# Kernel tuning notes

Measured on AMD Instinct MI355X. Metric: run time of the kernel, lower is better.

## Reference

```python
import jax, jax.numpy as jnp
import numpy as np

N_NODES = 100000
N_EDGES = 1600000
IN_C, HID_C, OUT_C = 128, 256, 47


def setup_inputs() -> dict:
    key = jax.random.key(0)
    ks = jax.random.split(key, 8)
    x = jax.random.normal(ks[0], (N_NODES, IN_C), dtype=jnp.float32)
    edge_index = jax.random.randint(ks[1], (2, N_EDGES), 0, N_NODES, dtype=jnp.int64)

    def glorot(k, fan_in, fan_out):
        s = 1.0 / np.sqrt(fan_in)
        return jax.random.uniform(k, (fan_in, fan_out), jnp.float32, -s, s)

    W1_l = glorot(ks[2], IN_C, HID_C)
    b1 = jnp.zeros((HID_C,), jnp.float32)
    W1_r = glorot(ks[3], IN_C, HID_C)
    W2_l = glorot(ks[4], HID_C, OUT_C)
    b2 = jnp.zeros((OUT_C,), jnp.float32)
    W2_r = glorot(ks[5], HID_C, OUT_C)
    return {"x": x, "edge_index": edge_index,
            "W1_l": W1_l, "b1": b1, "W1_r": W1_r,
            "W2_l": W2_l, "b2": b2, "W2_r": W2_r}


def _sage_conv(x, src, dst, W_l, b, W_r, num_nodes):
    # mean aggregation of source-node features onto destination nodes
    msg_sum = jax.ops.segment_sum(x[src], dst, num_segments=num_nodes)  # [N, C]
    cnt = jax.ops.segment_sum(jnp.ones((src.shape[0], 1), x.dtype), dst,
                              num_segments=num_nodes)                   # [N, 1]
    mean = msg_sum / jnp.maximum(cnt, 1.0)
    # out = lin_l(mean) + lin_r(x_root); lin_l carries the bias (PyG default)
    return mean @ W_l + b + x @ W_r


def reference(x, edge_index, W1_l, b1, W1_r, W2_l, b2, W2_r):
    num_nodes = x.shape[0]
    src, dst = edge_index[0], edge_index[1]
    h = _sage_conv(x, src, dst, W1_l, b1, W1_r, num_nodes)
    h = jax.nn.relu(h)  # dropout is identity in eval mode
    out = _sage_conv(h, src, dst, W2_l, b2, W2_r, num_nodes)
    return jax.nn.log_softmax(out, axis=-1)
```

## Files before the change

### kernel.cpp

```cpp
#include <hip/hip_runtime.h>
#include <hip/hip_bf16.h>

constexpr int IN_C  = 128;
constexpr int HID_C = 256;
constexpr int OUT_C = 47;
constexpr int CAP   = 64;

typedef __attribute__((ext_vector_type(8))) short bf16x8;
typedef __attribute__((ext_vector_type(4))) float f32x4;

static __device__ __forceinline__ unsigned short f2bf(float v) {
  __hip_bfloat16 hb = __float2bfloat16(v);
  return *(unsigned short*)&hb;
}
static __device__ __forceinline__ float bf2f(unsigned short u) {
  return __uint_as_float((unsigned)u << 16);
}

__global__ __launch_bounds__(256) void fill_bucket(const int* __restrict__ src,
                                                   const int* __restrict__ dst,
                                                   int* __restrict__ cursor,
                                                   int* __restrict__ csr,
                                                   int E, int lo, int hi) {
  int e = blockIdx.x * blockDim.x + threadIdx.x;
  const int stride = gridDim.x * blockDim.x;
  for (; e < E; e += stride) {
    const int d = __builtin_nontemporal_load(&dst[e]);
    if (d >= lo && d < hi) {
      const int s = __builtin_nontemporal_load(&src[e]);
      const int p = atomicAdd(&cursor[d], 1);
      if (p < CAP) csr[(size_t)d * CAP + p] = s;
    }
  }
}

__global__ void f32_to_bf16(const float* __restrict__ in, unsigned short* __restrict__ out, int n4) {
  int i = blockIdx.x * blockDim.x + threadIdx.x;
  if (i < n4) {
    float4 v = *(const float4*)&in[i * 4];
    ushort4 o;
    o.x = f2bf(v.x); o.y = f2bf(v.y); o.z = f2bf(v.z); o.w = f2bf(v.w);
    *(ushort4*)&out[i * 4] = o;
  }
}

__global__ void build_weights(const float* __restrict__ W1l, const float* __restrict__ W1r,
                              const float* __restrict__ W2l, const float* __restrict__ W2r,
                              unsigned short* __restrict__ W1T, unsigned short* __restrict__ W2T) {
  int idx = blockIdx.x * blockDim.x + threadIdx.x;
  if (idx < 256 * 256) {
    int j = idx >> 8, k = idx & 255;
    float v = (k < 128) ? W1l[k * 256 + j] : W1r[(k - 128) * 256 + j];
    W1T[idx] = f2bf(v);
  } else if (idx < 256 * 256 + 128 * 256) {
    int t = idx - 256 * 256;
    int j = t >> 8, k = t & 255;
    float v = 0.f;
    if (j < OUT_C)           v = W2l[k * OUT_C + j];
    else if (j < 2 * OUT_C)  v = W2r[k * OUT_C + (j - OUT_C)];
    W2T[t] = f2bf(v);
  }
}

__global__ __launch_bounds__(256) void agg1(const unsigned short* __restrict__ xb,
                                            const int* __restrict__ cursor,
                                            const int* __restrict__ csr,
                                            unsigned short* __restrict__ meanb, int N) {
  const int wid  = (blockIdx.x * blockDim.x + threadIdx.x) >> 6;
  const int lane = threadIdx.x & 63;
  if (wid >= N) return;
  const unsigned* xw = (const unsigned*)xb;
  const int degr = cursor[wid];
  const int deg  = min(degr, CAP);
  const int idx  = (lane < deg) ? csr[(size_t)wid * CAP + lane] : 0;
  float a0 = 0.f, a1 = 0.f, b0 = 0.f, b1 = 0.f;
  float c0 = 0.f, c1 = 0.f, d0 = 0.f, d1 = 0.f;
  int e = 0;
  for (; e + 4 <= deg; e += 4) {
    const int sA = __shfl(idx, e, 64),     sB = __shfl(idx, e + 1, 64);
    const int sC = __shfl(idx, e + 2, 64), sD = __shfl(idx, e + 3, 64);
    const unsigned uA = xw[(size_t)sA * 64 + lane];
    const unsigned uB = xw[(size_t)sB * 64 + lane];
    const unsigned uC = xw[(size_t)sC * 64 + lane];
    const unsigned uD = xw[(size_t)sD * 64 + lane];
    a0 += __uint_as_float(uA << 16); a1 += __uint_as_float(uA & 0xffff0000u);
    b0 += __uint_as_float(uB << 16); b1 += __uint_as_float(uB & 0xffff0000u);
    c0 += __uint_as_float(uC << 16); c1 += __uint_as_float(uC & 0xffff0000u);
    d0 += __uint_as_float(uD << 16); d1 += __uint_as_float(uD & 0xffff0000u);
  }
  for (; e < deg; ++e) {
    const int sA = __shfl(idx, e, 64);
    const unsigned uA = xw[(size_t)sA * 64 + lane];
    a0 += __uint_as_float(uA << 16); a1 += __uint_as_float(uA & 0xffff0000u);
  }
  const float r0 = (a0 + b0) + (c0 + d0);
  const float r1 = (a1 + b1) + (c1 + d1);
  const float inv = (degr > 0) ? 1.0f / (float)degr : 0.0f;
  const unsigned lo = f2bf(r0 * inv), hi = f2bf(r1 * inv);
  ((unsigned*)meanb)[(size_t)wid * 64 + lane] = lo | (hi << 16);
}

template<int MODE>
__global__ __launch_bounds__(256) void gemm_mfma(const unsigned short* __restrict__ A0,
                                                 const unsigned short* __restrict__ A1,
                                                 const unsigned short* __restrict__ BT,
                                                 const float* __restrict__ bias,
                                                 unsigned short* __restrict__ Out,
                                                 int M) {
  constexpr int ONC = (MODE == 0) ? 256 : 128;
  __shared__ unsigned short Asl[128 * 64];
  __shared__ unsigned short Bsl[128 * 64];
  const int tid  = threadIdx.x;
  const int wid  = tid >> 6, lane = tid & 63;
  const int wm   = wid >> 1, wn = wid & 1;
  const int r0   = blockIdx.x * 128;
  const int c0   = blockIdx.y * 128;

  f32x4 acc[4][4];
  #pragma unroll
  for (int m = 0; m < 4; ++m)
    #pragma unroll
    for (int n = 0; n < 4; ++n)
      #pragma unroll
      for (int j = 0; j < 4; ++j) acc[m][n][j] = 0.f;

  const int srow = lane >> 3;
  const int cs   = (lane & 7) ^ srow;
  const int fr   = lane & 15;
  const int klo  = (lane >> 4) * 16;
  const int swz  = (fr & 7) << 4;

  #pragma unroll 1
  for (int kb = 0; kb < 4; ++kb) {
    const unsigned short* Ap;
    int acol, ak;
    if (MODE == 0) { Ap = (kb < 2) ? A0 : A1; acol = (kb & 1) * 64; ak = 128; }
    else           { Ap = A0;                 acol = kb * 64;       ak = 256; }
    #pragma unroll
    for (int i = 0; i < 4; ++i) {
      const int rl = wid * 32 + i * 8 + srow;
      int gr = r0 + rl; if (gr > M - 1) gr = M - 1;
      const unsigned short* gsa = Ap + (size_t)gr * ak + acol + cs * 8;
      __builtin_amdgcn_global_load_lds(
          (const __attribute__((address_space(1))) unsigned int*)gsa,
          (__attribute__((address_space(3))) unsigned int*)&Asl[(wid * 32 + i * 8) * 64],
          16, 0, 0);
      const unsigned short* gsb = BT + (size_t)(c0 + rl) * 256 + kb * 64 + cs * 8;
      __builtin_amdgcn_global_load_lds(
          (const __attribute__((address_space(1))) unsigned int*)gsb,
          (__attribute__((address_space(3))) unsigned int*)&Bsl[(wid * 32 + i * 8) * 64],
          16, 0, 0);
    }
    asm volatile("s_waitcnt vmcnt(0)");
    __syncthreads();
    #pragma unroll
    for (int ks = 0; ks < 2; ++ks) {
      bf16x8 af[4], bfv[4];
      #pragma unroll
      for (int m = 0; m < 4; ++m) {
        const int ro = (wm * 64 + m * 16 + fr) * 128 + ((ks * 64 + klo) ^ swz);
        af[m] = *(const bf16x8*)((const char*)Asl + ro);
      }
      #pragma unroll
      for (int n = 0; n < 4; ++n) {
        const int ro = (wn * 64 + n * 16 + fr) * 128 + ((ks * 64 + klo) ^ swz);
        bfv[n] = *(const bf16x8*)((const char*)Bsl + ro);
      }
      #pragma unroll
      for (int m = 0; m < 4; ++m)
        #pragma unroll
        for (int n = 0; n < 4; ++n)
          acc[m][n] = __builtin_amdgcn_mfma_f32_16x16x32_bf16(af[m], bfv[n], acc[m][n], 0, 0, 0);
    }
    __syncthreads();
  }

  const int orow0 = r0 + wm * 64 + (lane >> 4) * 4;
  const int ocol0 = c0 + wn * 64 + (lane & 15);
  #pragma unroll
  for (int m = 0; m < 4; ++m) {
    #pragma unroll
    for (int n = 0; n < 4; ++n) {
      const int col = ocol0 + n * 16;
      const float badd = (MODE == 0) ? bias[col] : 0.f;
      #pragma unroll
      for (int j = 0; j < 4; ++j) {
        const int row = orow0 + m * 16 + j;
        if (row < M) {
          float v = acc[m][n][j] + badd;
          if (MODE == 0) v = fmaxf(v, 0.f);
          Out[(size_t)row * ONC + col] = f2bf(v);
        }
      }
    }
  }
}

__global__ __launch_bounds__(256) void final_kernel(const unsigned short* __restrict__ Ob,
                                                    const int* __restrict__ cursor,
                                                    const int* __restrict__ csr,
                                                    const float* __restrict__ b2,
                                                    float* __restrict__ out, int N) {
  const int wid  = (blockIdx.x * blockDim.x + threadIdx.x) >> 6;
  const int lane = threadIdx.x & 63;
  if (wid >= N) return;
  const int degr = cursor[wid];
  const int deg  = min(degr, CAP);
  const int idx  = (lane < deg) ? csr[(size_t)wid * CAP + lane] : 0;
  const bool act = lane < OUT_C;
  const int cl = act ? lane : 0;
  float t0 = 0.f, t1 = 0.f, t2 = 0.f, t3 = 0.f;
  int e = 0;
  for (; e + 4 <= deg; e += 4) {
    const int sA = __shfl(idx, e, 64),     sB = __shfl(idx, e + 1, 64);
    const int sC = __shfl(idx, e + 2, 64), sD = __shfl(idx, e + 3, 64);
    if (act) {
      t0 += bf2f(Ob[(size_t)sA * 128 + lane]);
      t1 += bf2f(Ob[(size_t)sB * 128 + lane]);
      t2 += bf2f(Ob[(size_t)sC * 128 + lane]);
      t3 += bf2f(Ob[(size_t)sD * 128 + lane]);
    }
  }
  for (; e < deg; ++e) {
    const int sA = __shfl(idx, e, 64);
    if (act) t0 += bf2f(Ob[(size_t)sA * 128 + lane]);
  }
  const float sum = (t0 + t1) + (t2 + t3);
  const float inv = (degr > 0) ? 1.0f / (float)degr : 0.0f;
  float v = sum * inv + b2[cl] + bf2f(Ob[(size_t)wid * 128 + OUT_C + cl]);
  if (!act) v = -INFINITY;
  float m = v;
  #pragma unroll
  for (int o = 32; o > 0; o >>= 1) m = fmaxf(m, __shfl_xor(m, o, 64));
  float ex = act ? expf(v - m) : 0.f;
  float s = ex;
  #pragma unroll
  for (int o = 32; o > 0; o >>= 1) s += __shfl_xor(s, o, 64);
  if (act) out[(size_t)wid * OUT_C + lane] = v - m - logf(s);
}


extern "C" void kernel_launch(void* const* d_in, const int* in_sizes, int n_in,
                              void* d_out, int out_size, void* d_ws, size_t ws_size,
                              hipStream_t stream) {
  const float* x   = (const float*)d_in[0];
  const int*   ei  = (const int*)d_in[1];
  const float* W1l = (const float*)d_in[2];
  const float* b1  = (const float*)d_in[3];
  const float* W1r = (const float*)d_in[4];
  const float* W2l = (const float*)d_in[5];
  const float* b2  = (const float*)d_in[6];
  const float* W2r = (const float*)d_in[7];
  float* out = (float*)d_out;

  const int N = in_sizes[0] / IN_C;
  const int E = in_sizes[1] / 2;
  const int* src = ei;
  const int* dst = ei + E;

  char* base = (char*)d_ws;
  size_t o = 0;
  auto take = [&](size_t bytes) -> char* {
    char* p = base + o;
    o = (o + bytes + 255) & ~(size_t)255;
    return p;
  };
  int* cursor = (int*)take((size_t)N * 4);
  const size_t zero_bytes = o;
  int* csr    = (int*)take((size_t)N * CAP * 4);
  unsigned short* xb    = (unsigned short*)take((size_t)N * IN_C * 2);
  unsigned short* meanb = (unsigned short*)take((size_t)N * IN_C * 2);
  unsigned short* h     = (unsigned short*)take((size_t)N * HID_C * 2);
  unsigned short* W1T   = (unsigned short*)take((size_t)256 * 256 * 2);
  unsigned short* W2T   = (unsigned short*)take((size_t)128 * 256 * 2);
  unsigned short* Ocat  = meanb;
  (void)ws_size; (void)n_in; (void)out_size;

  hipMemsetAsync(base, 0, zero_bytes, stream);

  const int tb = 256;

  const int P = 8;
  const int chunk = (N + P - 1) / P;
  for (int p = 0; p < P; ++p) {
    const int lo = p * chunk;
    const int hi = min(N, lo + chunk);
    fill_bucket<<<2048, tb, 0, stream>>>(src, dst, cursor, csr, E, lo, hi);
  }

  const int n4 = N * IN_C / 4;
  f32_to_bf16<<<(n4 + tb - 1) / tb, tb, 0, stream>>>(x, xb, n4);
  build_weights<<<384, 256, 0, stream>>>(W1l, W1r, W2l, W2r, W1T, W2T);

  agg1<<<(N + 3) / 4, 256, 0, stream>>>(xb, cursor, csr, meanb, N);

  const int mb = (N + 127) / 128;
  gemm_mfma<0><<<dim3(mb, 2), 256, 0, stream>>>(meanb, xb, W1T, b1, h, N);
  gemm_mfma<1><<<dim3(mb, 1), 256, 0, stream>>>(h, nullptr, W2T, nullptr, Ocat, N);

  final_kernel<<<(N + 3) / 4, 256, 0, stream>>>(Ocat, cursor, csr, b2, out, N);
}
```

Before: 425.6 us.

## Split layer-2 GEMM output into separate 64-wide arrays and unroll gathers by eight

The second GEMM now writes two 64-column arrays instead of one 128-wide array: the neighbour-projected part (W2_l) and the root part (W2_r). The W2 weight columns are re-laid out to match. The final gather now reads 128-byte rows from a compact array, which improves cache-line density for the random neighbour reads. Both gather loops (agg1 and final) are also unrolled to eight loads in flight, to raise memory-level parallelism at the cost of more registers.

Result: faster. 409.5 us (-3.8%).

```diff
diff --git a/kernel.cpp b/kernel.cpp
--- a/kernel.cpp
+++ b/kernel.cpp
@@ -16,6 +16,8 @@
 static __device__ __forceinline__ float bf2f(unsigned short u) {
   return __uint_as_float((unsigned)u << 16);
 }
+static __device__ __forceinline__ float lof(unsigned u) { return __uint_as_float(u << 16); }
+static __device__ __forceinline__ float hif(unsigned u) { return __uint_as_float(u & 0xffff0000u); }
 
 __global__ __launch_bounds__(256) void fill_bucket(const int* __restrict__ src,
                                                    const int* __restrict__ dst,
@@ -56,8 +58,8 @@
     int t = idx - 256 * 256;
     int j = t >> 8, k = t & 255;
     float v = 0.f;
-    if (j < OUT_C)           v = W2l[k * OUT_C + j];
-    else if (j < 2 * OUT_C)  v = W2r[k * OUT_C + (j - OUT_C)];
+    if (j < OUT_C)                     v = W2l[k * OUT_C + j];
+    else if (j >= 64 && j < 64 + OUT_C) v = W2r[k * OUT_C + (j - 64)];
     W2T[t] = f2bf(v);
   }
 }
@@ -76,28 +78,38 @@
   float a0 = 0.f, a1 = 0.f, b0 = 0.f, b1 = 0.f;
   float c0 = 0.f, c1 = 0.f, d0 = 0.f, d1 = 0.f;
   int e = 0;
+  for (; e + 8 <= deg; e += 8) {
+    const int s0 = __shfl(idx, e, 64),     s1 = __shfl(idx, e + 1, 64);
+    const int s2 = __shfl(idx, e + 2, 64), s3 = __shfl(idx, e + 3, 64);
+    const int s4 = __shfl(idx, e + 4, 64), s5 = __shfl(idx, e + 5, 64);
+    const int s6 = __shfl(idx, e + 6, 64), s7 = __shfl(idx, e + 7, 64);
+    const unsigned u0 = xw[(size_t)s0 * 64 + lane], u1 = xw[(size_t)s1 * 64 + lane];
+    const unsigned u2 = xw[(size_t)s2 * 64 + lane], u3 = xw[(size_t)s3 * 64 + lane];
+    const unsigned u4 = xw[(size_t)s4 * 64 + lane], u5 = xw[(size_t)s5 * 64 + lane];
+    const unsigned u6 = xw[(size_t)s6 * 64 + lane], u7 = xw[(size_t)s7 * 64 + lane];
+    a0 += lof(u0); a1 += hif(u0); b0 += lof(u1); b1 += hif(u1);
+    c0 += lof(u2); c1 += hif(u2); d0 += lof(u3); d1 += hif(u3);
+    a0 += lof(u4); a1 += hif(u4); b0 += lof(u5); b1 += hif(u5);
+    c0 += lof(u6); c1 += hif(u6); d0 += lof(u7); d1 += hif(u7);
+  }
   for (; e + 4 <= deg; e += 4) {
-    const int sA = __shfl(idx, e, 64),     sB = __shfl(idx, e + 1, 64);
-    const int sC = __shfl(idx, e + 2, 64), sD = __shfl(idx, e + 3, 64);
-    const unsigned uA = xw[(size_t)sA * 64 + lane];
-    const unsigned uB = xw[(size_t)sB * 64 + lane];
-    const unsigned uC = xw[(size_t)sC * 64 + lane];
-    const unsigned uD = xw[(size_t)sD * 64 + lane];
-    a0 += __uint_as_float(uA << 16); a1 += __uint_as_float(uA & 0xffff0000u);
-    b0 += __uint_as_float(uB << 16); b1 += __uint_as_float(uB & 0xffff0000u);
-    c0 += __uint_as_float(uC << 16); c1 += __uint_as_float(uC & 0xffff0000u);
-    d0 += __uint_as_float(uD << 16); d1 += __uint_as_float(uD & 0xffff0000u);
+    const int s0 = __shfl(idx, e, 64),     s1 = __shfl(idx, e + 1, 64);
+    const int s2 = __shfl(idx, e + 2, 64), s3 = __shfl(idx, e + 3, 64);
+    const unsigned u0 = xw[(size_t)s0 * 64 + lane], u1 = xw[(size_t)s1 * 64 + lane];
+    const unsigned u2 = xw[(size_t)s2 * 64 + lane], u3 = xw[(size_t)s3 * 64 + lane];
+    a0 += lof(u0); a1 += hif(u0); b0 += lof(u1); b1 += hif(u1);
+    c0 += lof(u2); c1 += hif(u2); d0 += lof(u3); d1 += hif(u3);
   }
   for (; e < deg; ++e) {
-    const int sA = __shfl(idx, e, 64);
-    const unsigned uA = xw[(size_t)sA * 64 + lane];
-    a0 += __uint_as_float(uA << 16); a1 += __uint_as_float(uA & 0xffff0000u);
+    const int s0 = __shfl(idx, e, 64);
+    const unsigned u0 = xw[(size_t)s0 * 64 + lane];
+    a0 += lof(u0); a1 += hif(u0);
   }
   const float r0 = (a0 + b0) + (c0 + d0);
   const float r1 = (a1 + b1) + (c1 + d1);
   const float inv = (degr > 0) ? 1.0f / (float)degr : 0.0f;
-  const unsigned lo = f2bf(r0 * inv), hi = f2bf(r1 * inv);
-  ((unsigned*)meanb)[(size_t)wid * 64 + lane] = lo | (hi << 16);
+  const unsigned wlo = f2bf(r0 * inv), whi = f2bf(r1 * inv);
+  ((unsigned*)meanb)[(size_t)wid * 64 + lane] = wlo | (whi << 16);
 }
 
 template<int MODE>
@@ -106,8 +118,8 @@
                                                  const unsigned short* __restrict__ BT,
                                                  const float* __restrict__ bias,
                                                  unsigned short* __restrict__ Out,
+                                                 unsigned short* __restrict__ OutR,
                                                  int M) {
-  constexpr int ONC = (MODE == 0) ? 256 : 128;
   __shared__ unsigned short Asl[128 * 64];
   __shared__ unsigned short Bsl[128 * 64];
   const int tid  = threadIdx.x;
@@ -188,15 +200,21 @@
         const int row = orow0 + m * 16 + j;
         if (row < M) {
           float v = acc[m][n][j] + badd;
-          if (MODE == 0) v = fmaxf(v, 0.f);
-          Out[(size_t)row * ONC + col] = f2bf(v);
+          if (MODE == 0) {
+            v = fmaxf(v, 0.f);
+            Out[(size_t)row * HID_C + col] = f2bf(v);
+          } else {
+            if (col < 64) Out[(size_t)row * 64 + col] = f2bf(v);
+            else          OutR[(size_t)row * 64 + (col - 64)] = f2bf(v);
+          }
         }
       }
     }
   }
 }
 
-__global__ __launch_bounds__(256) void final_kernel(const unsigned short* __restrict__ Ob,
+__global__ __launch_bounds__(256) void final_kernel(const unsigned short* __restrict__ Ol,
+                                                    const unsigned short* __restrict__ Or,
                                                     const int* __restrict__ cursor,
                                                     const int* __restrict__ csr,
                                                     const float* __restrict__ b2,
@@ -211,23 +229,39 @@
   const int cl = act ? lane : 0;
   float t0 = 0.f, t1 = 0.f, t2 = 0.f, t3 = 0.f;
   int e = 0;
+  for (; e + 8 <= deg; e += 8) {
+    const int s0 = __shfl(idx, e, 64),     s1 = __shfl(idx, e + 1, 64);
+    const int s2 = __shfl(idx, e + 2, 64), s3 = __shfl(idx, e + 3, 64);
+    const int s4 = __shfl(idx, e + 4, 64), s5 = __shfl(idx, e + 5, 64);
+    const int s6 = __shfl(idx, e + 6, 64), s7 = __shfl(idx, e + 7, 64);
+    if (act) {
+      t0 += bf2f(Ol[(size_t)s0 * 64 + lane]);
+      t1 += bf2f(Ol[(size_t)s1 * 64 + lane]);
+      t2 += bf2f(Ol[(size_t)s2 * 64 + lane]);
+      t3 += bf2f(Ol[(size_t)s3 * 64 + lane]);
+      t0 += bf2f(Ol[(size_t)s4 * 64 + lane]);
+      t1 += bf2f(Ol[(size_t)s5 * 64 + lane]);
+      t2 += bf2f(Ol[(size_t)s6 * 64 + lane]);
+      t3 += bf2f(Ol[(size_t)s7 * 64 + lane]);
+    }
+  }
   for (; e + 4 <= deg; e += 4) {
-    const int sA = __shfl(idx, e, 64),     sB = __shfl(idx, e + 1, 64);
-    const int sC = __shfl(idx, e + 2, 64), sD = __shfl(idx, e + 3, 64);
+    const int s0 = __shfl(idx, e, 64),     s1 = __shfl(idx, e + 1, 64);
+    const int s2 = __shfl(idx, e + 2, 64), s3 = __shfl(idx, e + 3, 64);
     if (act) {
-      t0 += bf2f(Ob[(size_t)sA * 128 + lane]);
-      t1 += bf2f(Ob[(size_t)sB * 128 + lane]);
-      t2 += bf2f(Ob[(size_t)sC * 128 + lane]);
-      t3 += bf2f(Ob[(size_t)sD * 128 + lane]);
+      t0 += bf2f(Ol[(size_t)s0 * 64 + lane]);
+      t1 += bf2f(Ol[(size_t)s1 * 64 + lane]);
+      t2 += bf2f(Ol[(size_t)s2 * 64 + lane]);
+      t3 += bf2f(Ol[(size_t)s3 * 64 + lane]);
     }
   }
   for (; e < deg; ++e) {
-    const int sA = __shfl(idx, e, 64);
-    if (act) t0 += bf2f(Ob[(size_t)sA * 128 + lane]);
+    const int s0 = __shfl(idx, e, 64);
+    if (act) t0 += bf2f(Ol[(size_t)s0 * 64 + lane]);
   }
   const float sum = (t0 + t1) + (t2 + t3);
   const float inv = (degr > 0) ? 1.0f / (float)degr : 0.0f;
-  float v = sum * inv + b2[cl] + bf2f(Ob[(size_t)wid * 128 + OUT_C + cl]);
+  float v = sum * inv + b2[cl] + bf2f(Or[(size_t)wid * 64 + cl]);
   if (!act) v = -INFINITY;
   float m = v;
   #pragma unroll
@@ -273,7 +307,8 @@
   unsigned short* h     = (unsigned short*)take((size_t)N * HID_C * 2);
   unsigned short* W1T   = (unsigned short*)take((size_t)256 * 256 * 2);
   unsigned short* W2T   = (unsigned short*)take((size_t)128 * 256 * 2);
-  unsigned short* Ocat  = meanb;
+  unsigned short* Ol    = meanb;
+  unsigned short* Or    = meanb + (size_t)N * 64;
   (void)ws_size; (void)n_in; (void)out_size;
 
   hipMemsetAsync(base, 0, zero_bytes, stream);
@@ -295,8 +330,8 @@
   agg1<<<(N + 3) / 4, 256, 0, stream>>>(xb, cursor, csr, meanb, N);
 
   const int mb = (N + 127) / 128;
-  gemm_mfma<0><<<dim3(mb, 2), 256, 0, stream>>>(meanb, xb, W1T, b1, h, N);
-  gemm_mfma<1><<<dim3(mb, 1), 256, 0, stream>>>(h, nullptr, W2T, nullptr, Ocat, N);
-
-  final_kernel<<<(N + 3) / 4, 256, 0, stream>>>(Ocat, cursor, csr, b2, out, N);
-}
+  gemm_mfma<0><<<dim3(mb, 2), 256, 0, stream>>>(meanb, xb, W1T, b1, h, nullptr, N);
+  gemm_mfma<1><<<dim3(mb, 1), 256, 0, stream>>>(h, nullptr, W2T, nullptr, Ol, Or, N);
+
+  final_kernel<<<(N + 3) / 4, 256, 0, stream>>>(Ol, Or, cursor, csr, b2, out, N);
+}
```
